# Optimization experiments

Measured on AMD Instinct MI355X. Metric: run time of the kernel, lower is better.

Reference implementation:

```python
import jax, jax.numpy as jnp
import numpy as np

OBS_LEN = 20
N_COORD = 2
HIDDEN = 1024  # z_dim + c_dim = 512 + 512
N = 4096


def setup_inputs() -> dict:
    key = jax.random.key(0)
    ks = jax.random.split(key, 6)
    obs_traj_rel = jax.random.normal(ks[0], (OBS_LEN, N, N_COORD), dtype=jnp.float32)
    pred_lstm_hidden = jax.random.normal(ks[1], (N, HIDDEN), dtype=jnp.float32)
    # LSTMCell params (PyTorch layout): weight_ih [4H, in], weight_hh [4H, H],
    # initialized N(0, 0.1); biases zero (per _initialize_weights).
    W_ih = 0.1 * jax.random.normal(ks[2], (4 * HIDDEN, N_COORD), dtype=jnp.float32)
    W_hh = 0.1 * jax.random.normal(ks[3], (4 * HIDDEN, HIDDEN), dtype=jnp.float32)
    b_ih = jnp.zeros((4 * HIDDEN,), dtype=jnp.float32)
    b_hh = jnp.zeros((4 * HIDDEN,), dtype=jnp.float32)
    # hidden2pos Linear: weight [n_coord, H], bias zero
    W_out = 0.1 * jax.random.normal(ks[4], (N_COORD, HIDDEN), dtype=jnp.float32)
    b_out = jnp.zeros((N_COORD,), dtype=jnp.float32)
    return {
        "obs_traj_rel": obs_traj_rel,
        "pred_lstm_hidden": pred_lstm_hidden,
        "W_ih": W_ih,
        "W_hh": W_hh,
        "b_ih": b_ih,
        "b_hh": b_hh,
        "W_out": W_out,
        "b_out": b_out,
        "variant_feats": 1,
    }


def reference(obs_traj_rel, pred_lstm_hidden, W_ih, W_hh, b_ih, b_hh, W_out, b_out, variant_feats):
    # Step 0 consumes obs[0]; step i>=1 consumes obs[i-1] (per the original loop).
    x_seq = jnp.concatenate([obs_traj_rel[:1], obs_traj_rel[:-1]], axis=0)[..., :N_COORD]
    c0 = jnp.zeros_like(pred_lstm_hidden)

    def step(carry, x_t):
        h, c = carry
        # PyTorch LSTMCell: gates = x W_ih^T + b_ih + h W_hh^T + b_hh, order i,f,g,o
        gates = x_t @ W_ih.T + b_ih + h @ W_hh.T + b_hh
        i, f, g, o = jnp.split(gates, 4, axis=-1)
        c = jax.nn.sigmoid(f) * c + jax.nn.sigmoid(i) * jnp.tanh(g)
        h = jax.nn.sigmoid(o) * jnp.tanh(c)
        out = h @ W_out.T + b_out  # [N, n_coord]
        return (h, c), out

    _, outs = jax.lax.scan(step, (pred_lstm_hidden, c0), x_seq)
    return outs  # [obs_len, N, n_coord]
```

## Files before the change

### kernel.cpp

```cpp
#include <hip/hip_runtime.h>
#include <hip/hip_bf16.h>
#include <stdint.h>

#define N_BATCH 4096
#define HID     1024
#define OBSLEN  20

#define BM  128
#define BHC 32
#define BK  64

using short8 = __attribute__((ext_vector_type(8))) short;
using f32x4  = __attribute__((ext_vector_type(4))) float;

__device__ __forceinline__ float rcpf(float x) { return __builtin_amdgcn_rcpf(x); }
__device__ __forceinline__ float sigf(float x) { return rcpf(1.f + __expf(-x)); }
__device__ __forceinline__ float tanh_(float x) {
    float a = fminf(15.f, fmaxf(-15.f, x));
    float t = __expf(-2.f * a);
    return (1.f - t) * rcpf(1.f + t);
}
__device__ __forceinline__ unsigned short f2bf(float f) {
    __hip_bfloat16 b = __float2bfloat16(f);
    return *reinterpret_cast<unsigned short*>(&b);
}
__device__ __forceinline__ float bf2f(unsigned short u) {
    unsigned int x = ((unsigned int)u) << 16;
    return __uint_as_float(x);
}

__global__ __launch_bounds__(256) void prep_kernel(
    const float4* __restrict__ Whh, const float4* __restrict__ h0,
    ushort4* __restrict__ Wg, ushort4* __restrict__ hb, float4* __restrict__ c, int n4)
{
    int i = blockIdx.x * 256 + threadIdx.x;
    if (i < n4) {
        float4 w = Whh[i];
        float4 h = h0[i];
        Wg[i] = make_ushort4(f2bf(w.x), f2bf(w.y), f2bf(w.z), f2bf(w.w));
        hb[i] = make_ushort4(f2bf(h.x), f2bf(h.y), f2bf(h.z), f2bf(h.w));
        c[i] = make_float4(0.f, 0.f, 0.f, 0.f);
    }
}

__global__ __launch_bounds__(256, 2) void lstm_step_kernel(
    const ushort* __restrict__ hin,
    const ushort* __restrict__ Wg,
    const float*  __restrict__ xt,
    const float*  __restrict__ Wih,
    const float*  __restrict__ bih,
    const float*  __restrict__ bhh,
    float*        __restrict__ cst,
    ushort*       __restrict__ hout)
{
    __shared__ __align__(16) char lds[65536];
    const int tid  = threadIdx.x;
    const int wid  = tid >> 6, lane = tid & 63;
    const int l15  = lane & 15, l4 = lane >> 4;
    const int m0   = blockIdx.x * BM;
    const int h0c  = blockIdx.y * BHC;
    const int wr   = wid >> 1, wc = wid & 1;

    const int rowS = tid >> 3;
    const int offS = ((tid & 7) * 16) ^ ((rowS & 7) << 4);
    const ushort* aSrc0 = hin + (size_t)(m0 + rowS) * HID + (offS >> 1);
    const ushort* bSrc0 = Wg  + (size_t)(h0c + rowS) * HID + (offS >> 1);

    auto stage = [&](int buf, int k0) {
        char* ab = lds + buf * 32768 + tid * 16;
        char* bb = ab + 16384;
        const ushort* as = aSrc0 + k0;
        const ushort* bs = bSrc0 + k0;
#pragma unroll
        for (int r = 0; r < 4; ++r) {
            __builtin_amdgcn_global_load_lds(
                (const __attribute__((address_space(1))) void*)(as + (size_t)r * 32 * HID),
                (__attribute__((address_space(3))) void*)(ab + r * 4096), 16, 0, 0);
            __builtin_amdgcn_global_load_lds(
                (const __attribute__((address_space(1))) void*)(bs + (size_t)r * 1024 * HID),
                (__attribute__((address_space(3))) void*)(bb + r * 4096), 16, 0, 0);
        }
    };

    f32x4 acc[4][4];
#pragma unroll
    for (int a = 0; a < 4; ++a)
#pragma unroll
        for (int b = 0; b < 4; ++b)
            acc[a][b] = (f32x4){0.f, 0.f, 0.f, 0.f};

    stage(0, 0);
    __syncthreads();

    const int swz = (l15 & 7) << 4;
    const int NK = HID / BK;
    for (int kt = 0; kt < NK; ++kt) {
        const int cur = kt & 1;
        if (kt < NK - 1) stage(cur ^ 1, (kt + 1) * BK);

        const char* A = lds + cur * 32768;
        const char* B = A + 16384;
#pragma unroll
        for (int kk = 0; kk < 2; ++kk) {
            const int kb = (kk * 64 + l4 * 16) ^ swz;
            short8 af[4], bfr[4];
#pragma unroll
            for (int fr = 0; fr < 4; ++fr) {
                int row = wr * 64 + fr * 16 + l15;
                af[fr] = *(const short8*)(A + row * 128 + kb);
            }
#pragma unroll
            for (int g = 0; g < 4; ++g) {
                int hc = wc * 16 + l15;
                bfr[g] = *(const short8*)(B + g * 4096 + hc * 128 + kb);
            }
#pragma unroll
            for (int fr = 0; fr < 4; ++fr)
#pragma unroll
                for (int g = 0; g < 4; ++g)
                    acc[fr][g] = __builtin_amdgcn_mfma_f32_16x16x32_bf16(af[fr], bfr[g], acc[fr][g], 0, 0, 0);
        }
        __syncthreads();
    }

    const int hcg = h0c + wc * 16 + l15;
    float wi0[4], wi1[4], bs_[4];
#pragma unroll
    for (int g = 0; g < 4; ++g) {
        int j = g * HID + hcg;
        wi0[g] = Wih[j * 2 + 0];
        wi1[g] = Wih[j * 2 + 1];
        bs_[g] = bih[j] + bhh[j];
    }
#pragma unroll
    for (int fr = 0; fr < 4; ++fr) {
#pragma unroll
        for (int r = 0; r < 4; ++r) {
            int n = m0 + wr * 64 + fr * 16 + l4 * 4 + r;
            float x0 = xt[n * 2 + 0], x1 = xt[n * 2 + 1];
            float gi = acc[fr][0][r] + x0 * wi0[0] + x1 * wi1[0] + bs_[0];
            float gf = acc[fr][1][r] + x0 * wi0[1] + x1 * wi1[1] + bs_[1];
            float gg = acc[fr][2][r] + x0 * wi0[2] + x1 * wi1[2] + bs_[2];
            float go = acc[fr][3][r] + x0 * wi0[3] + x1 * wi1[3] + bs_[3];
            float iv = sigf(gi), fv = sigf(gf);
            float gv = tanh_(gg), ov = sigf(go);
            size_t idx = (size_t)n * HID + hcg;
            float cn = fv * cst[idx] + iv * gv;
            cst[idx]  = cn;
            hout[idx] = f2bf(ov * tanh_(cn));
        }
    }
}

__global__ __launch_bounds__(256) void out_proj_kernel(
    const ushort* __restrict__ h, const float* __restrict__ Wout,
    const float* __restrict__ bout, float* __restrict__ outt)
{
    const int wid = threadIdx.x >> 6, lane = threadIdx.x & 63;
    const int row = blockIdx.x * 4 + wid;
    const ushort* hr = h + (size_t)row * HID + lane * 16;
    float a0 = 0.f, a1 = 0.f;
#pragma unroll
    for (int half = 0; half < 2; ++half) {
        short8 hv = *(const short8*)(hr + half * 8);
#pragma unroll
        for (int j = 0; j < 8; ++j) {
            int k = lane * 16 + half * 8 + j;
            float f = bf2f((unsigned short)hv[j]);
            a0 += f * Wout[k];
            a1 += f * Wout[HID + k];
        }
    }
#pragma unroll
    for (int off = 32; off > 0; off >>= 1) {
        a0 += __shfl_down(a0, off);
        a1 += __shfl_down(a1, off);
    }
    if (lane == 0) {
        outt[row * 2 + 0] = a0 + bout[0];
        outt[row * 2 + 1] = a1 + bout[1];
    }
}

extern "C" void kernel_launch(void* const* d_in, const int* in_sizes, int n_in,
                              void* d_out, int out_size, void* d_ws, size_t ws_size,
                              hipStream_t stream) {
    const float* obs  = (const float*)d_in[0];
    const float* h0   = (const float*)d_in[1];
    const float* Wih  = (const float*)d_in[2];
    const float* Whh  = (const float*)d_in[3];
    const float* bih  = (const float*)d_in[4];
    const float* bhh  = (const float*)d_in[5];
    const float* Wout = (const float*)d_in[6];
    const float* bout = (const float*)d_in[7];
    float* out = (float*)d_out;

    char* ws = (char*)d_ws;
    ushort* Wg = (ushort*)(ws);
    ushort* hA = (ushort*)(ws + (8  << 20));
    ushort* hB = (ushort*)(ws + (16 << 20));
    float*  c  = (float* )(ws + (24 << 20));

    prep_kernel<<<4096, 256, 0, stream>>>((const float4*)Whh, (const float4*)h0,
                                          (ushort4*)Wg, (ushort4*)hA, (float4*)c,
                                          N_BATCH * HID / 4);

    ushort* hin = hA;
    ushort* hou = hB;
    for (int t = 0; t < OBSLEN; ++t) {
        const float* xt = obs + (size_t)(t == 0 ? 0 : (t - 1)) * N_BATCH * 2;
        lstm_step_kernel<<<dim3(N_BATCH / BM, HID / BHC), 256, 0, stream>>>(
            hin, Wg, xt, Wih, bih, bhh, c, hou);
        out_proj_kernel<<<N_BATCH / 4, 256, 0, stream>>>(
            hou, Wout, bout, out + (size_t)t * N_BATCH * 2);
        ushort* tmp = hin; hin = hou; hou = tmp;
    }
}
```

Measured before the change: 988.1 us.

## Enlarge LSTM GEMM tiles to 256x64 with interleaved staged loads and priority hints

Each block now covers 256 batch rows by 64 hidden columns (256 gate columns) with 512 threads, 8 waves and 128 KB of LDS. The reduction loop splits each K tile into four MFMA phases. Each phase issues part of the next tile's global-to-LDS loads and waits on them with explicit vmcnt counts instead of a full barrier per tile, and s_setprio is raised around the MFMA bursts. The goal is more operand reuse per LDS byte and better overlap of memory traffic with MFMA work. The cost is much higher register and LDS use, which limits the GPU to one block per CU and gives a grid of exactly 256 blocks.

```diff
diff --git a/kernel.cpp b/kernel.cpp
--- a/kernel.cpp
+++ b/kernel.cpp
@@ -6,12 +6,15 @@
 #define HID     1024
 #define OBSLEN  20
 
-#define BM  128
-#define BHC 32
+#define BM  256
+#define BHC 64
 #define BK  64
 
 using short8 = __attribute__((ext_vector_type(8))) short;
 using f32x4  = __attribute__((ext_vector_type(4))) float;
+
+#define AS1 __attribute__((address_space(1)))
+#define AS3 __attribute__((address_space(3)))
 
 __device__ __forceinline__ float rcpf(float x) { return __builtin_amdgcn_rcpf(x); }
 __device__ __forceinline__ float sigf(float x) { return rcpf(1.f + __expf(-x)); }
@@ -43,7 +46,7 @@
     }
 }
 
-__global__ __launch_bounds__(256, 2) void lstm_step_kernel(
+__global__ __launch_bounds__(512, 2) void lstm_step_kernel(
     const ushort* __restrict__ hin,
     const ushort* __restrict__ Wg,
     const float*  __restrict__ xt,
@@ -53,74 +56,112 @@
     float*        __restrict__ cst,
     ushort*       __restrict__ hout)
 {
-    __shared__ __align__(16) char lds[65536];
+    __shared__ __align__(16) char lds[131072];
     const int tid  = threadIdx.x;
-    const int wid  = tid >> 6, lane = tid & 63;
-    const int l15  = lane & 15, l4 = lane >> 4;
+    const int lane = tid & 63, l15 = lane & 15, l4 = lane >> 4;
+    const int wid  = tid >> 6, wr = wid >> 2, wc = wid & 3;
     const int m0   = blockIdx.x * BM;
     const int h0c  = blockIdx.y * BHC;
-    const int wr   = wid >> 1, wc = wid & 1;
 
     const int rowS = tid >> 3;
     const int offS = ((tid & 7) * 16) ^ ((rowS & 7) << 4);
-    const ushort* aSrc0 = hin + (size_t)(m0 + rowS) * HID + (offS >> 1);
-    const ushort* bSrc0 = Wg  + (size_t)(h0c + rowS) * HID + (offS >> 1);
-
-    auto stage = [&](int buf, int k0) {
-        char* ab = lds + buf * 32768 + tid * 16;
-        char* bb = ab + 16384;
-        const ushort* as = aSrc0 + k0;
-        const ushort* bs = bSrc0 + k0;
-#pragma unroll
-        for (int r = 0; r < 4; ++r) {
-            __builtin_amdgcn_global_load_lds(
-                (const __attribute__((address_space(1))) void*)(as + (size_t)r * 32 * HID),
-                (__attribute__((address_space(3))) void*)(ab + r * 4096), 16, 0, 0);
-            __builtin_amdgcn_global_load_lds(
-                (const __attribute__((address_space(1))) void*)(bs + (size_t)r * 1024 * HID),
-                (__attribute__((address_space(3))) void*)(bb + r * 4096), 16, 0, 0);
-        }
+    const ushort* aS = hin + (size_t)(m0 + rowS) * HID + (offS >> 1);
+    const ushort* bS = Wg  + (size_t)(h0c + rowS) * HID + (offS >> 1);
+    char* aD = lds + tid * 16;
+    char* bD = lds + 65536 + tid * 16;
+
+    auto stA = [&](int buf, int kt1, int r) {
+        __builtin_amdgcn_global_load_lds(
+            (const AS1 void*)(aS + kt1 * BK + (size_t)r * 64 * HID),
+            (AS3 void*)(aD + buf * 32768 + r * 8192), 16, 0, 0);
     };
-
-    f32x4 acc[4][4];
-#pragma unroll
-    for (int a = 0; a < 4; ++a)
-#pragma unroll
-        for (int b = 0; b < 4; ++b)
-            acc[a][b] = (f32x4){0.f, 0.f, 0.f, 0.f};
-
-    stage(0, 0);
-    __syncthreads();
-
-    const int swz = (l15 & 7) << 4;
+    auto stB = [&](int buf, int kt1, int r) {
+        __builtin_amdgcn_global_load_lds(
+            (const AS1 void*)(bS + kt1 * BK + (size_t)r * 1024 * HID),
+            (AS3 void*)(bD + buf * 32768 + r * 8192), 16, 0, 0);
+    };
+
+    const int swz  = (l15 & 7) << 4;
+    const int aOff = (wr * 128 + l15) * 128 + ((l4 * 16) ^ swz);
+    const int bOff = (wc * 16  + l15) * 128 + ((l4 * 16) ^ swz);
+
+    f32x4 acc[8][4];
+#pragma unroll
+    for (int f = 0; f < 8; ++f)
+#pragma unroll
+        for (int g = 0; g < 4; ++g)
+            acc[f][g] = (f32x4){0.f, 0.f, 0.f, 0.f};
+
+#pragma unroll
+    for (int r = 0; r < 4; ++r) stA(0, 0, r);
+#pragma unroll
+    for (int r = 0; r < 4; ++r) stB(0, 0, r);
+
     const int NK = HID / BK;
     for (int kt = 0; kt < NK; ++kt) {
-        const int cur = kt & 1;
-        if (kt < NK - 1) stage(cur ^ 1, (kt + 1) * BK);
-
+        const int cur = kt & 1, nxt = cur ^ 1;
+        const bool st = (kt < NK - 1);
         const char* A = lds + cur * 32768;
-        const char* B = A + 16384;
-#pragma unroll
-        for (int kk = 0; kk < 2; ++kk) {
-            const int kb = (kk * 64 + l4 * 16) ^ swz;
-            short8 af[4], bfr[4];
-#pragma unroll
-            for (int fr = 0; fr < 4; ++fr) {
-                int row = wr * 64 + fr * 16 + l15;
-                af[fr] = *(const short8*)(A + row * 128 + kb);
-            }
-#pragma unroll
-            for (int g = 0; g < 4; ++g) {
-                int hc = wc * 16 + l15;
-                bfr[g] = *(const short8*)(B + g * 4096 + hc * 128 + kb);
-            }
-#pragma unroll
-            for (int fr = 0; fr < 4; ++fr)
-#pragma unroll
-                for (int g = 0; g < 4; ++g)
-                    acc[fr][g] = __builtin_amdgcn_mfma_f32_16x16x32_bf16(af[fr], bfr[g], acc[fr][g], 0, 0, 0);
-        }
-        __syncthreads();
+        const char* B = lds + 65536 + cur * 32768;
+
+        short8 af[8], bf0, bf1, bf2, bf3;
+
+        asm volatile("s_waitcnt vmcnt(2)" ::: "memory");
+        __builtin_amdgcn_s_barrier();
+        __builtin_amdgcn_sched_barrier(0);
+#pragma unroll
+        for (int f = 0; f < 8; ++f)
+            af[f] = *(const short8*)(A + aOff + f * 2048);
+        bf0 = *(const short8*)(B + bOff);
+        bf1 = *(const short8*)(B + bOff + 8192);
+        if (st) { stA(nxt, kt + 1, 0); stA(nxt, kt + 1, 1); }
+        __builtin_amdgcn_s_setprio(1);
+#pragma unroll
+        for (int f = 0; f < 8; ++f) {
+            acc[f][0] = __builtin_amdgcn_mfma_f32_16x16x32_bf16(af[f], bf0, acc[f][0], 0, 0, 0);
+            acc[f][1] = __builtin_amdgcn_mfma_f32_16x16x32_bf16(af[f], bf1, acc[f][1], 0, 0, 0);
+        }
+        __builtin_amdgcn_s_setprio(0);
+
+        if (st) asm volatile("s_waitcnt vmcnt(2)" ::: "memory");
+        else    asm volatile("s_waitcnt vmcnt(0)" ::: "memory");
+        __builtin_amdgcn_s_barrier();
+        __builtin_amdgcn_sched_barrier(0);
+        bf2 = *(const short8*)(B + bOff + 16384);
+        bf3 = *(const short8*)(B + bOff + 24576);
+        if (st) { stA(nxt, kt + 1, 2); stA(nxt, kt + 1, 3); }
+        __builtin_amdgcn_s_setprio(1);
+#pragma unroll
+        for (int f = 0; f < 8; ++f) {
+            acc[f][2] = __builtin_amdgcn_mfma_f32_16x16x32_bf16(af[f], bf2, acc[f][2], 0, 0, 0);
+            acc[f][3] = __builtin_amdgcn_mfma_f32_16x16x32_bf16(af[f], bf3, acc[f][3], 0, 0, 0);
+        }
+        __builtin_amdgcn_s_setprio(0);
+
+#pragma unroll
+        for (int f = 0; f < 8; ++f)
+            af[f] = *(const short8*)(A + (aOff ^ 64) + f * 2048);
+        bf0 = *(const short8*)(B + (bOff ^ 64));
+        bf1 = *(const short8*)(B + (bOff ^ 64) + 8192);
+        if (st) { stB(nxt, kt + 1, 0); stB(nxt, kt + 1, 1); }
+        __builtin_amdgcn_s_setprio(1);
+#pragma unroll
+        for (int f = 0; f < 8; ++f) {
+            acc[f][0] = __builtin_amdgcn_mfma_f32_16x16x32_bf16(af[f], bf0, acc[f][0], 0, 0, 0);
+            acc[f][1] = __builtin_amdgcn_mfma_f32_16x16x32_bf16(af[f], bf1, acc[f][1], 0, 0, 0);
+        }
+        __builtin_amdgcn_s_setprio(0);
+
+        bf2 = *(const short8*)(B + (bOff ^ 64) + 16384);
+        bf3 = *(const short8*)(B + (bOff ^ 64) + 24576);
+        if (st) { stB(nxt, kt + 1, 2); stB(nxt, kt + 1, 3); }
+        __builtin_amdgcn_s_setprio(1);
+#pragma unroll
+        for (int f = 0; f < 8; ++f) {
+            acc[f][2] = __builtin_amdgcn_mfma_f32_16x16x32_bf16(af[f], bf2, acc[f][2], 0, 0, 0);
+            acc[f][3] = __builtin_amdgcn_mfma_f32_16x16x32_bf16(af[f], bf3, acc[f][3], 0, 0, 0);
+        }
+        __builtin_amdgcn_s_setprio(0);
     }
 
     const int hcg = h0c + wc * 16 + l15;
@@ -133,15 +174,15 @@
         bs_[g] = bih[j] + bhh[j];
     }
 #pragma unroll
-    for (int fr = 0; fr < 4; ++fr) {
+    for (int f = 0; f < 8; ++f) {
 #pragma unroll
         for (int r = 0; r < 4; ++r) {
-            int n = m0 + wr * 64 + fr * 16 + l4 * 4 + r;
+            int n = m0 + wr * 128 + f * 16 + l4 * 4 + r;
             float x0 = xt[n * 2 + 0], x1 = xt[n * 2 + 1];
-            float gi = acc[fr][0][r] + x0 * wi0[0] + x1 * wi1[0] + bs_[0];
-            float gf = acc[fr][1][r] + x0 * wi0[1] + x1 * wi1[1] + bs_[1];
-            float gg = acc[fr][2][r] + x0 * wi0[2] + x1 * wi1[2] + bs_[2];
-            float go = acc[fr][3][r] + x0 * wi0[3] + x1 * wi1[3] + bs_[3];
+            float gi = acc[f][0][r] + x0 * wi0[0] + x1 * wi1[0] + bs_[0];
+            float gf = acc[f][1][r] + x0 * wi0[1] + x1 * wi1[1] + bs_[1];
+            float gg = acc[f][2][r] + x0 * wi0[2] + x1 * wi1[2] + bs_[2];
+            float go = acc[f][3][r] + x0 * wi0[3] + x1 * wi1[3] + bs_[3];
             float iv = sigf(gi), fv = sigf(gf);
             float gv = tanh_(gg), ov = sigf(go);
             size_t idx = (size_t)n * HID + hcg;
@@ -209,7 +250,7 @@
     ushort* hou = hB;
     for (int t = 0; t < OBSLEN; ++t) {
         const float* xt = obs + (size_t)(t == 0 ? 0 : (t - 1)) * N_BATCH * 2;
-        lstm_step_kernel<<<dim3(N_BATCH / BM, HID / BHC), 256, 0, stream>>>(
+        lstm_step_kernel<<<dim3(N_BATCH / BM, HID / BHC), 512, 0, stream>>>(
             hin, Wg, xt, Wih, bih, bhh, c, hou);
         out_proj_kernel<<<N_BATCH / 4, 256, 0, stream>>>(
             hou, Wout, bout, out + (size_t)t * N_BATCH * 2);
```

Measured after the change: 892.4 us. -9.7%, faster.
